# Optimization experiments

Measured on AMD Instinct MI355X. Metric: run time of the kernel, lower is better.

## Reference

```python
import jax, jax.numpy as jnp
import numpy as np

H = W = 32
C = 512
RED = 16


def make_gus(v=1.5):
    # gus[p=(i,k), x, y] = exp(-((x-i)^2+(y-k)^2)/(2 v^2)) / (2 pi v^2), normalized per p.
    idx = np.arange(H, dtype=np.float64)
    d2 = (idx[:, None] - idx[None, :]) ** 2          # [center, coord]
    g1 = np.exp(-d2 / (2.0 * v * v))                  # separable factor
    g = np.einsum('ix,ky->ikxy', g1, g1) / (2.0 * np.pi * v * v)
    g = g / g.sum(axis=(2, 3), keepdims=True)         # per-position normalization
    return jnp.asarray(g.reshape(H * W, H, W), dtype=jnp.float32)


def setup_inputs() -> dict:
    key = jax.random.key(0)
    ks = jax.random.split(key, 6)
    b = 16
    return {
        'x': jax.random.normal(ks[0], (b, C, H, W), dtype=jnp.float32),
        'se_w1': jax.random.normal(ks[1], (C // RED, C), dtype=jnp.float32) * 0.02,
        'se_b1': jnp.zeros((C // RED,), dtype=jnp.float32),
        'se_w2': jax.random.normal(ks[2], (C, C // RED), dtype=jnp.float32) * 0.02,
        'se_b2': jnp.zeros((C,), dtype=jnp.float32),
        'down_w': jax.random.normal(ks[3], (C, 2 * C), dtype=jnp.float32) * 0.02,
        'gus': make_gus(1.5),
    }


def _patches3(img, h, w):
    # img: [b, c, h+2, w+2] -> [b, c, h, w, 9] (3x3 neighborhoods, row-major dy*3+dx)
    ps = [img[:, :, dy:dy + h, dx:dx + w] for dy in range(3) for dx in range(3)]
    return jnp.stack(ps, axis=-1)


def reference(x, se_w1, se_b1, se_w2, se_b2, down_w, gus):
    b, c, h, w = x.shape
    # --- SELayer ---
    s = x.mean(axis=(2, 3))                                   # [b, c]
    y = jax.nn.relu(s @ se_w1.T + se_b1)                       # [b, c/16]
    y = jax.nn.sigmoid(y @ se_w2.T + se_b2)                    # [b, c]
    out32 = x * y[:, :, None, None]
    # --- gaussian-weighted global pooling per output position ---
    # g[b, p, ch] = sum_{y,x} gus[p,y,x] * out32[b,ch,y,x]; then torch's view(c,h,w)
    gus_out = jnp.einsum('pyx,bcyx->bpc', gus, out32).reshape(b, c, h, w)
    # --- patch self-attention ---
    sig = jax.nn.sigmoid(out32)
    sigp = _patches3(jnp.pad(sig, ((0, 0), (0, 0), (1, 1), (1, 1))), h, w)    # [b,c,h,w,9]
    ffp = _patches3(jnp.pad(out32, ((0, 0), (0, 0), (1, 1), (1, 1))), h, w)   # [b,c,h,w,9]
    logits = jnp.einsum('bcyx,bcyxk->byxk', sig, sigp) / c     # mean over channels
    attn = jax.nn.softmax(logits, axis=-1)                     # softmax over 3x3 patch
    g2 = jnp.einsum('byxk,bcyxk->byxc', attn, ffp)             # [b,h,w,c] = [b, p, c]
    out_csa = g2.reshape(b, c, h, w)                           # torch view(c,h,w) of [hw,c]
    # --- down: 1x1 conv (no bias) + InstanceNorm2d + LeakyReLU(0.2) ---
    cat = jnp.concatenate([gus_out, out_csa], axis=1)          # [b, 2c, h, w]
    z = jnp.einsum('oi,biyx->boyx', down_w, cat)
    mu = z.mean(axis=(2, 3), keepdims=True)
    var = z.var(axis=(2, 3), keepdims=True)
    zn = (z - mu) * jax.lax.rsqrt(var + 1e-5)
    return jnp.where(zn >= 0, zn, 0.2 * zn)
```

## Files before the change

### kernel.cpp

```cpp
#include <hip/hip_runtime.h>
#include <stdint.h>

#define NB 16
#define NC 512
#define NS 1024
#define NR 32

typedef unsigned short u16;
typedef unsigned int u32;

typedef __attribute__((ext_vector_type(8))) short short8;
typedef __attribute__((ext_vector_type(4))) float f32x4;

__device__ __forceinline__ float bf2f(u16 u) {
    union { u32 i; float f; } c; c.i = ((u32)u) << 16; return c.f;
}
__device__ __forceinline__ u16 f2bf(float f) {
    union { float f; u32 i; } c; c.f = f;
    u32 r = (c.i + 0x7FFFu + ((c.i >> 16) & 1u)) >> 16;
    return (u16)r;
}
__device__ __forceinline__ float sigm(float x) {
    return 1.0f / (1.0f + __expf(-x));
}

__global__ void k_mean(const float* __restrict__ x, float* __restrict__ sm) {
    const int row = blockIdx.x;
    const float4* xr = (const float4*)(x + (long)row * NS);
    const int t = threadIdx.x;
    float4 v = xr[t];
    float p = v.x + v.y + v.z + v.w;
    for (int off = 32; off; off >>= 1) p += __shfl_down(p, off);
    __shared__ float red[4];
    if ((t & 63) == 0) red[t >> 6] = p;
    __syncthreads();
    if (t == 0) sm[row] = (red[0] + red[1] + red[2] + red[3]) * (1.0f / 1024.0f);
}

__global__ void k_se(const float* __restrict__ sm, const float* __restrict__ w1,
                     const float* __restrict__ b1, const float* __restrict__ w2,
                     const float* __restrict__ b2, float* __restrict__ y) {
    const int b = blockIdx.x;
    __shared__ float s_s[NC];
    __shared__ float s_y1[NR];
    const int t = threadIdx.x;
    s_s[t] = sm[b * NC + t];
    s_s[t + 256] = sm[b * NC + t + 256];
    __syncthreads();
    if (t < NR) {
        float acc = b1[t];
        for (int c = 0; c < NC; ++c) acc += s_s[c] * w1[t * NC + c];
        s_y1[t] = fmaxf(acc, 0.0f);
    }
    __syncthreads();
    for (int i = 0; i < 2; ++i) {
        int c = t + i * 256;
        float acc = b2[c];
#pragma unroll
        for (int r = 0; r < NR; ++r) acc += s_y1[r] * w2[c * NR + r];
        y[b * NC + c] = 1.0f / (1.0f + expf(-acc));
    }
}

__global__ void k_scale(const float* __restrict__ x, const float* __restrict__ y,
                        u16* __restrict__ o32, u16* __restrict__ o32t,
                        u16* __restrict__ sig_t) {
    const int b = blockIdx.z;
    const int c0 = blockIdx.y * 32;
    const int s0 = blockIdx.x * 32;
    const int tx = threadIdx.x & 31, ty = threadIdx.x >> 5;
    __shared__ float tile[32][33];
    const float* xb = x + (long)b * NC * NS;
#pragma unroll
    for (int it = 0; it < 4; ++it) {
        int c = c0 + ty + it * 8;
        float v = xb[(long)c * NS + s0 + tx] * y[b * NC + c];
        tile[ty + it * 8][tx] = v;
        o32[((long)b * NC + c) * NS + s0 + tx] = f2bf(v);
    }
    __syncthreads();
#pragma unroll
    for (int it = 0; it < 4; ++it) {
        int sr = ty + it * 8;
        float tv = tile[tx][sr];
        long idx = ((long)b * NS + (s0 + sr)) * NC + c0 + tx;
        o32t[idx] = f2bf(tv);
        sig_t[idx] = f2bf(sigm(tv));
    }
}

__global__ void k_cvt(const float* __restrict__ g, const float* __restrict__ dw,
                      u16* __restrict__ gb, u16* __restrict__ dwb) {
    const int i = blockIdx.x * 256 + threadIdx.x;
    gb[i] = f2bf(g[i]);
    if (i < 524288) dwb[i] = f2bf(dw[i]);
}

__device__ __forceinline__ void st_out(float* p, float v) { *p = v; }
__device__ __forceinline__ void st_out(u16* p, float v) { *p = f2bf(v); }

template <typename OT>
__global__ __launch_bounds__(256)
void gemm_bt(const u16* __restrict__ A, const u16* __restrict__ Bt, OT* __restrict__ Co,
             int M, int N, int K, long batA, long batB, long batC) {
    const int b = blockIdx.z;
    const u16* Ab = A + (long)b * batA;
    const u16* Bb = Bt + (long)b * batB;
    OT* Cb = Co + (long)b * batC;
    const int m0 = blockIdx.y * 128, n0 = blockIdx.x * 128;
    __shared__ __align__(16) u16 As[128 * 64];
    __shared__ __align__(16) u16 Bs[128 * 64];
    const int tid = threadIdx.x;
    const int lane = tid & 63, wave = tid >> 6;
    const int wm = (wave >> 1) * 64, wn = (wave & 1) * 64;
    f32x4 acc[4][4];
#pragma unroll
    for (int i = 0; i < 4; ++i)
#pragma unroll
        for (int j = 0; j < 4; ++j) acc[i][j] = (f32x4){0.f, 0.f, 0.f, 0.f};

    int mrow[4], kcol[4];
#pragma unroll
    for (int q = 0; q < 4; ++q) {
        int eoff = wave * 2048 + q * 512 + lane * 8;
        mrow[q] = eoff >> 6;
        kcol[q] = eoff & 63;
    }

    for (int k0 = 0; k0 < K; k0 += 64) {
#pragma unroll
        for (int q = 0; q < 4; ++q) {
            const u16* ga = Ab + (long)(m0 + mrow[q]) * K + (k0 + kcol[q]);
            __builtin_amdgcn_global_load_lds(
                (const __attribute__((address_space(1))) u32*)ga,
                (__attribute__((address_space(3))) u32*)&As[wave * 2048 + q * 512], 16, 0, 0);
            const u16* gb = Bb + (long)(n0 + mrow[q]) * K + (k0 + kcol[q]);
            __builtin_amdgcn_global_load_lds(
                (const __attribute__((address_space(1))) u32*)gb,
                (__attribute__((address_space(3))) u32*)&Bs[wave * 2048 + q * 512], 16, 0, 0);
        }
        __syncthreads();
#pragma unroll
        for (int kk = 0; kk < 64; kk += 32) {
            const int kidx = kk + ((lane >> 4) << 3);
            short8 af[4], bfr[4];
#pragma unroll
            for (int i = 0; i < 4; ++i)
                af[i] = *(const short8*)&As[(wm + i * 16 + (lane & 15)) * 64 + kidx];
#pragma unroll
            for (int j = 0; j < 4; ++j)
                bfr[j] = *(const short8*)&Bs[(wn + j * 16 + (lane & 15)) * 64 + kidx];
#pragma unroll
            for (int i = 0; i < 4; ++i)
#pragma unroll
                for (int j = 0; j < 4; ++j)
                    acc[i][j] = __builtin_amdgcn_mfma_f32_16x16x32_bf16(af[i], bfr[j], acc[i][j], 0, 0, 0);
        }
        __syncthreads();
    }
    const int col = lane & 15, rq = (lane >> 4) * 4;
#pragma unroll
    for (int i = 0; i < 4; ++i)
#pragma unroll
        for (int j = 0; j < 4; ++j)
#pragma unroll
            for (int r = 0; r < 4; ++r) {
                int row = m0 + wm + i * 16 + rq + r;
                int ncol = n0 + wn + j * 16 + col;
                st_out(&Cb[(long)row * N + ncol], acc[i][j][r]);
            }
}

__global__ __launch_bounds__(256)
void k_attn(const u16* __restrict__ sig_t, const u16* __restrict__ o32t,
            u16* __restrict__ g2) {
    const int wave = threadIdx.x >> 6, lane = threadIdx.x & 63;
    const int s = blockIdx.x * 4 + wave;
    const int b = blockIdx.y;
    const int y0 = s >> 5, x0 = s & 31;
    const long base = (long)b * NS * NC;
    const int coff = lane * 8;

    short8 csv = *(const short8*)&sig_t[base + (long)s * NC + coff];
    float sc[8];
#pragma unroll
    for (int j = 0; j < 8; ++j) sc[j] = bf2f((u16)csv[j]);

    float part[9];
    short8 raw[9];
#pragma unroll
    for (int k = 0; k < 9; ++k) {
        int yy = y0 + k / 3 - 1, xx = x0 + k % 3 - 1;
        bool valid = (yy >= 0 && yy < 32 && xx >= 0 && xx < 32);
        if (valid) {
            long roff = base + (long)(yy * 32 + xx) * NC + coff;
            short8 sv = *(const short8*)&sig_t[roff];
            raw[k] = *(const short8*)&o32t[roff];
            float p = 0.f;
#pragma unroll
            for (int j = 0; j < 8; ++j) p += sc[j] * bf2f((u16)sv[j]);
            part[k] = p;
        } else {
            raw[k] = (short8){0, 0, 0, 0, 0, 0, 0, 0};
            part[k] = 0.f;
        }
    }
#pragma unroll
    for (int k = 0; k < 9; ++k)
        for (int off = 32; off; off >>= 1) part[k] += __shfl_down(part[k], off);

    if (lane == 0) {
        float mx = -1e30f;
#pragma unroll
        for (int k = 0; k < 9; ++k) { part[k] *= (1.0f / 512.0f); mx = fmaxf(mx, part[k]); }
        float sum = 0.f;
#pragma unroll
        for (int k = 0; k < 9; ++k) { part[k] = __expf(part[k] - mx); sum += part[k]; }
        float inv = 1.0f / sum;
#pragma unroll
        for (int k = 0; k < 9; ++k) part[k] *= inv;
    }
    float g[8] = {0.f, 0.f, 0.f, 0.f, 0.f, 0.f, 0.f, 0.f};
#pragma unroll
    for (int k = 0; k < 9; ++k) {
        float a = __shfl(part[k], 0);
#pragma unroll
        for (int j = 0; j < 8; ++j) g[j] += a * bf2f((u16)raw[k][j]);
    }
    short8 ov;
#pragma unroll
    for (int j = 0; j < 8; ++j) ov[j] = (short)f2bf(g[j]);
    *(short8*)&g2[base + (long)s * NC + coff] = ov;
}

__global__ void k_tr(const u16* __restrict__ g, const u16* __restrict__ g2,
                     u16* __restrict__ ct) {
    const int b = blockIdx.z;
    const int i0 = blockIdx.y * 32, s0 = blockIdx.x * 32;
    const int tx = threadIdx.x & 31, ty = threadIdx.x >> 5;
    __shared__ u16 tile[32][33];
    const u16* src = (i0 < 512) ? (g + (long)b * 524288 + (long)i0 * 1024)
                                : (g2 + (long)b * 524288 + (long)(i0 - 512) * 1024);
#pragma unroll
    for (int it = 0; it < 4; ++it) {
        int il = ty + it * 8;
        tile[il][tx] = src[(long)il * 1024 + s0 + tx];
    }
    __syncthreads();
#pragma unroll
    for (int it = 0; it < 4; ++it) {
        int sl = ty + it * 8;
        ct[(long)b * 1048576 + (long)(s0 + sl) * 1024 + i0 + tx] = tile[tx][sl];
    }
}

__global__ void k_norm(const float* __restrict__ z, float* __restrict__ out) {
    const int row = blockIdx.x;
    const float4* zr = (const float4*)(z + (long)row * NS);
    const int t = threadIdx.x;
    float4 v = zr[t];
    float sm = v.x + v.y + v.z + v.w;
    float sq = v.x * v.x + v.y * v.y + v.z * v.z + v.w * v.w;
    for (int off = 32; off; off >>= 1) { sm += __shfl_down(sm, off); sq += __shfl_down(sq, off); }
    __shared__ float rs[4], rq2[4];
    if ((t & 63) == 0) { rs[t >> 6] = sm; rq2[t >> 6] = sq; }
    __syncthreads();
    float tot = rs[0] + rs[1] + rs[2] + rs[3];
    float totq = rq2[0] + rq2[1] + rq2[2] + rq2[3];
    float mu = tot * (1.0f / 1024.0f);
    float var = totq * (1.0f / 1024.0f) - mu * mu;
    float sc = rsqrtf(var + 1e-5f);
    float4 o;
    float a;
    a = (v.x - mu) * sc; o.x = (a >= 0.f) ? a : 0.2f * a;
    a = (v.y - mu) * sc; o.y = (a >= 0.f) ? a : 0.2f * a;
    a = (v.z - mu) * sc; o.z = (a >= 0.f) ? a : 0.2f * a;
    a = (v.w - mu) * sc; o.w = (a >= 0.f) ? a : 0.2f * a;
    ((float4*)(out + (long)row * NS))[t] = o;
}

extern "C" void kernel_launch(void* const* d_in, const int* in_sizes, int n_in,
                              void* d_out, int out_size, void* d_ws, size_t ws_size,
                              hipStream_t stream) {
    const float* x   = (const float*)d_in[0];
    const float* w1  = (const float*)d_in[1];
    const float* b1  = (const float*)d_in[2];
    const float* w2  = (const float*)d_in[3];
    const float* b2  = (const float*)d_in[4];
    const float* dw  = (const float*)d_in[5];
    const float* gus = (const float*)d_in[6];
    float* out = (float*)d_out;
    char* ws = (char*)d_ws;

    float* sm_buf = (float*)(ws + 0);
    float* y_buf  = (float*)(ws + 32768);
    u16* gusbf    = (u16*)(ws + 65536);
    u16* dwbf     = (u16*)(ws + 2162688);
    char* regA    = ws + 3211264;
    u16* o32      = (u16*)regA;
    u16* o32t     = (u16*)(regA + 16777216);
    u16* catT     = (u16*)regA;
    char* regB    = ws + 36765696;
    u16* sig_t    = (u16*)regB;
    u16* gbuf     = (u16*)regB;
    u16* g2b      = (u16*)(regB + 16777216);
    float* Z      = (float*)regB;

    k_mean<<<dim3(NB * NC), dim3(256), 0, stream>>>(x, sm_buf);
    k_se<<<dim3(NB), dim3(256), 0, stream>>>(sm_buf, w1, b1, w2, b2, y_buf);
    k_scale<<<dim3(32, 16, NB), dim3(256), 0, stream>>>(x, y_buf, o32, o32t, sig_t);
    k_cvt<<<dim3(4096), dim3(256), 0, stream>>>(gus, dw, gusbf, dwbf);
    k_attn<<<dim3(256, NB), dim3(256), 0, stream>>>(sig_t, o32t, g2b);
    gemm_bt<u16><<<dim3(4, 8, NB), dim3(256), 0, stream>>>(
        gusbf, o32, gbuf, 1024, 512, 1024, 0L, (long)NC * NS, (long)NC * NS);
    k_tr<<<dim3(32, 32, NB), dim3(256), 0, stream>>>(gbuf, g2b, catT);
    gemm_bt<float><<<dim3(8, 4, NB), dim3(256), 0, stream>>>(
        dwbf, catT, Z, 512, 1024, 1024, 0L, (long)NS * 1024, (long)NC * NS);
    k_norm<<<dim3(NB * NC), dim3(256), 0, stream>>>(Z, out);
}
```

Measured before the change: 224.9 us.

## Shrink GEMM N-tile to 64 and stage attention neighborhoods in LDS

The batched GEMM now uses 128x64 tiles with 4-wave occupancy hints, which doubles the block count so the device has more blocks to schedule. Each wave computes fewer MFMA tiles, and the B operand is reloaded more often. The attention kernel now cooperatively loads the 3x6 neighborhood of sig and out32 rows into LDS once per block of 4 adjacent pixels. This replaces the 9 separate global loads each wave made and reuses overlapping neighbors, at the cost of about 36KB of LDS per block.

```diff
diff --git a/kernel.cpp b/kernel.cpp
--- a/kernel.cpp
+++ b/kernel.cpp
@@ -100,60 +100,58 @@
 __device__ __forceinline__ void st_out(u16* p, float v) { *p = f2bf(v); }
 
 template <typename OT>
-__global__ __launch_bounds__(256)
+__global__ __launch_bounds__(256, 4)
 void gemm_bt(const u16* __restrict__ A, const u16* __restrict__ Bt, OT* __restrict__ Co,
              int M, int N, int K, long batA, long batB, long batC) {
     const int b = blockIdx.z;
     const u16* Ab = A + (long)b * batA;
     const u16* Bb = Bt + (long)b * batB;
     OT* Cb = Co + (long)b * batC;
-    const int m0 = blockIdx.y * 128, n0 = blockIdx.x * 128;
+    const int m0 = blockIdx.y * 128, n0 = blockIdx.x * 64;
     __shared__ __align__(16) u16 As[128 * 64];
-    __shared__ __align__(16) u16 Bs[128 * 64];
+    __shared__ __align__(16) u16 Bs[64 * 64];
     const int tid = threadIdx.x;
     const int lane = tid & 63, wave = tid >> 6;
-    const int wm = (wave >> 1) * 64, wn = (wave & 1) * 64;
-    f32x4 acc[4][4];
+    const int wm = (wave >> 1) * 64, wn = (wave & 1) * 32;
+    f32x4 acc[4][2];
 #pragma unroll
     for (int i = 0; i < 4; ++i)
 #pragma unroll
-        for (int j = 0; j < 4; ++j) acc[i][j] = (f32x4){0.f, 0.f, 0.f, 0.f};
-
-    int mrow[4], kcol[4];
-#pragma unroll
-    for (int q = 0; q < 4; ++q) {
-        int eoff = wave * 2048 + q * 512 + lane * 8;
-        mrow[q] = eoff >> 6;
-        kcol[q] = eoff & 63;
-    }
+        for (int j = 0; j < 2; ++j) acc[i][j] = (f32x4){0.f, 0.f, 0.f, 0.f};
+
+    const int erow = (tid * 8) >> 6;
+    const int ecol = (tid * 8) & 63;
 
     for (int k0 = 0; k0 < K; k0 += 64) {
 #pragma unroll
         for (int q = 0; q < 4; ++q) {
-            const u16* ga = Ab + (long)(m0 + mrow[q]) * K + (k0 + kcol[q]);
+            const u16* ga = Ab + (long)(m0 + q * 32 + erow) * K + (k0 + ecol);
             __builtin_amdgcn_global_load_lds(
                 (const __attribute__((address_space(1))) u32*)ga,
-                (__attribute__((address_space(3))) u32*)&As[wave * 2048 + q * 512], 16, 0, 0);
-            const u16* gb = Bb + (long)(n0 + mrow[q]) * K + (k0 + kcol[q]);
+                (__attribute__((address_space(3))) u32*)&As[q * 2048 + tid * 8], 16, 0, 0);
+        }
+#pragma unroll
+        for (int q = 0; q < 2; ++q) {
+            const u16* gb = Bb + (long)(n0 + q * 32 + erow) * K + (k0 + ecol);
             __builtin_amdgcn_global_load_lds(
                 (const __attribute__((address_space(1))) u32*)gb,
-                (__attribute__((address_space(3))) u32*)&Bs[wave * 2048 + q * 512], 16, 0, 0);
+                (__attribute__((address_space(3))) u32*)&Bs[q * 2048 + tid * 8], 16, 0, 0);
         }
         __syncthreads();
 #pragma unroll
         for (int kk = 0; kk < 64; kk += 32) {
             const int kidx = kk + ((lane >> 4) << 3);
-            short8 af[4], bfr[4];
+            short8 af[4], bfr[2];
 #pragma unroll
             for (int i = 0; i < 4; ++i)
                 af[i] = *(const short8*)&As[(wm + i * 16 + (lane & 15)) * 64 + kidx];
 #pragma unroll
-            for (int j = 0; j < 4; ++j)
+            for (int j = 0; j < 2; ++j)
                 bfr[j] = *(const short8*)&Bs[(wn + j * 16 + (lane & 15)) * 64 + kidx];
 #pragma unroll
             for (int i = 0; i < 4; ++i)
 #pragma unroll
-                for (int j = 0; j < 4; ++j)
+                for (int j = 0; j < 2; ++j)
                     acc[i][j] = __builtin_amdgcn_mfma_f32_16x16x32_bf16(af[i], bfr[j], acc[i][j], 0, 0, 0);
         }
         __syncthreads();
@@ -162,7 +160,7 @@
 #pragma unroll
     for (int i = 0; i < 4; ++i)
 #pragma unroll
-        for (int j = 0; j < 4; ++j)
+        for (int j = 0; j < 2; ++j)
 #pragma unroll
             for (int r = 0; r < 4; ++r) {
                 int row = m0 + wm + i * 16 + rq + r;
@@ -175,35 +173,49 @@
 void k_attn(const u16* __restrict__ sig_t, const u16* __restrict__ o32t,
             u16* __restrict__ g2) {
     const int wave = threadIdx.x >> 6, lane = threadIdx.x & 63;
-    const int s = blockIdx.x * 4 + wave;
+    const int tid = threadIdx.x;
+    const int bx = blockIdx.x;
     const int b = blockIdx.y;
-    const int y0 = s >> 5, x0 = s & 31;
+    const int y0 = bx >> 3;
+    const int xbase = (bx & 7) * 4;
     const long base = (long)b * NS * NC;
+    __shared__ __align__(16) u16 smem[2 * 18 * NC];
+
+#pragma unroll
+    for (int r = 0; r < 9; ++r) {
+        int idx = r * 256 + tid;
+        int pair = idx >> 7;
+        int rem = idx & 127;
+        int arr = rem >> 6;
+        int ch0 = (rem & 63) * 8;
+        int yy = y0 + pair / 6 - 1;
+        int xx = xbase + pair % 6 - 1;
+        short8 v;
+        if (yy >= 0 && yy < 32 && xx >= 0 && xx < 32) {
+            long roff = base + (long)(yy * 32 + xx) * NC + ch0;
+            v = arr ? *(const short8*)&o32t[roff] : *(const short8*)&sig_t[roff];
+        } else {
+            v = (short8){0, 0, 0, 0, 0, 0, 0, 0};
+        }
+        *(short8*)&smem[(arr * 18 + pair) * NC + ch0] = v;
+    }
+    __syncthreads();
+
     const int coff = lane * 8;
-
-    short8 csv = *(const short8*)&sig_t[base + (long)s * NC + coff];
+    short8 csv = *(const short8*)&smem[(6 + wave + 1) * NC + coff];
     float sc[8];
 #pragma unroll
     for (int j = 0; j < 8; ++j) sc[j] = bf2f((u16)csv[j]);
 
     float part[9];
-    short8 raw[9];
 #pragma unroll
     for (int k = 0; k < 9; ++k) {
-        int yy = y0 + k / 3 - 1, xx = x0 + k % 3 - 1;
-        bool valid = (yy >= 0 && yy < 32 && xx >= 0 && xx < 32);
-        if (valid) {
-            long roff = base + (long)(yy * 32 + xx) * NC + coff;
-            short8 sv = *(const short8*)&sig_t[roff];
-            raw[k] = *(const short8*)&o32t[roff];
-            float p = 0.f;
-#pragma unroll
-            for (int j = 0; j < 8; ++j) p += sc[j] * bf2f((u16)sv[j]);
-            part[k] = p;
-        } else {
-            raw[k] = (short8){0, 0, 0, 0, 0, 0, 0, 0};
-            part[k] = 0.f;
-        }
+        int pair = (k / 3) * 6 + wave + k % 3;
+        short8 sv = *(const short8*)&smem[pair * NC + coff];
+        float p = 0.f;
+#pragma unroll
+        for (int j = 0; j < 8; ++j) p += sc[j] * bf2f((u16)sv[j]);
+        part[k] = p;
     }
 #pragma unroll
     for (int k = 0; k < 9; ++k)
@@ -224,12 +236,15 @@
 #pragma unroll
     for (int k = 0; k < 9; ++k) {
         float a = __shfl(part[k], 0);
-#pragma unroll
-        for (int j = 0; j < 8; ++j) g[j] += a * bf2f((u16)raw[k][j]);
+        int pair = (k / 3) * 6 + wave + k % 3;
+        short8 rv = *(const short8*)&smem[(18 + pair) * NC + coff];
+#pragma unroll
+        for (int j = 0; j < 8; ++j) g[j] += a * bf2f((u16)rv[j]);
     }
     short8 ov;
 #pragma unroll
     for (int j = 0; j < 8; ++j) ov[j] = (short)f2bf(g[j]);
+    const int s = y0 * 32 + xbase + wave;
     *(short8*)&g2[base + (long)s * NC + coff] = ov;
 }
 
@@ -311,10 +326,10 @@
     k_scale<<<dim3(32, 16, NB), dim3(256), 0, stream>>>(x, y_buf, o32, o32t, sig_t);
     k_cvt<<<dim3(4096), dim3(256), 0, stream>>>(gus, dw, gusbf, dwbf);
     k_attn<<<dim3(256, NB), dim3(256), 0, stream>>>(sig_t, o32t, g2b);
-    gemm_bt<u16><<<dim3(4, 8, NB), dim3(256), 0, stream>>>(
+    gemm_bt<u16><<<dim3(8, 8, NB), dim3(256), 0, stream>>>(
         gusbf, o32, gbuf, 1024, 512, 1024, 0L, (long)NC * NS, (long)NC * NS);
     k_tr<<<dim3(32, 32, NB), dim3(256), 0, stream>>>(gbuf, g2b, catT);
-    gemm_bt<float><<<dim3(8, 4, NB), dim3(256), 0, stream>>>(
+    gemm_bt<float><<<dim3(16, 4, NB), dim3(256), 0, stream>>>(
         dwbf, catT, Z, 512, 1024, 1024, 0L, (long)NS * 1024, (long)NC * NS);
     k_norm<<<dim3(NB * NC), dim3(256), 0, stream>>>(Z, out);
 }
```

After: 231.9 us. +3.1%, slower.
